# Kernel tuning notes

Measured on AMD Instinct MI355X. Metric: run time of the kernel, lower is better.

## Reference

```python
import jax, jax.numpy as jnp
import numpy as np

N = 100000      # nodes
E = 1_600_000   # edges (avg degree 16)
IN, HID, OUT = 64, 64, 32


def setup_inputs() -> dict:
    key = jax.random.key(0)
    k1, k2, k3, k4, k5, k6 = jax.random.split(key, 6)
    x = jax.random.uniform(k1, (N, IN), dtype=jnp.float32)
    edge_index = jax.random.randint(k2, (2, E), 0, N, dtype=jnp.int32)
    # GCNConv weights (glorot-ish scale) and biases
    W1 = jax.random.normal(k3, (IN, HID), dtype=jnp.float32) * (1.0 / np.sqrt(IN))
    b1 = jnp.zeros((HID,), dtype=jnp.float32)
    W2 = jax.random.normal(k4, (HID, OUT), dtype=jnp.float32) * (1.0 / np.sqrt(HID))
    b2 = jnp.zeros((OUT,), dtype=jnp.float32)
    return {"x": x, "edge_index": edge_index, "W1": W1, "b1": b1, "W2": W2, "b2": b2}


def reference(x, edge_index, W1, b1, W2, b2):
    n = x.shape[0]
    # PyG GCNConv: add self-loops, symmetric deg^{-1/2} normalization
    loops = jnp.arange(n, dtype=edge_index.dtype)
    src = jnp.concatenate([edge_index[0], loops])  # message sources
    dst = jnp.concatenate([edge_index[1], loops])  # message targets
    ones = jnp.ones(src.shape[0], dtype=x.dtype)
    deg = jax.ops.segment_sum(ones, dst, num_segments=n)
    dinv = jnp.where(deg > 0, jax.lax.rsqrt(deg), 0.0)
    norm = dinv[src] * dinv[dst]  # [E+N]

    def gcn_conv(h, W, b):
        h = h @ W                          # [n, d_out]
        msg = h[src] * norm[:, None]       # gather + edge-normalize
        agg = jax.ops.segment_sum(msg, dst, num_segments=n)  # scatter-add
        return agg + b

    h = jax.nn.relu(gcn_conv(x, W1, b1))
    return gcn_conv(h, W2, b2)
```

## Files before the change

kernel.cpp:

```cpp
#include <hip/hip_runtime.h>
#include <hip/hip_fp16.h>


#define BSHIFT 8
#define BNODES 256
#define NB 256
#define CAP 5120

union H8 {
    uint4 u;
    __half2 h[4];
};

__device__ inline float2 u2f2(unsigned u) {
    union { unsigned x; __half2 h; } c;
    c.x = u;
    return __half22float2(c.h);
}
__device__ inline unsigned f2u(float a, float b) {
    union { unsigned x; __half2 h; } c;
    c.h = __floats2half2_rn(a, b);
    return c.x;
}

__global__ __launch_bounds__(256) void scatter_kernel(
    const int* __restrict__ src, const int* __restrict__ dst,
    int* __restrict__ cur, int* __restrict__ buf, int E) {
    __shared__ int h[512];
    __shared__ int curl[512];
    int t = threadIdx.x, b = blockIdx.x;
    for (int i = t; i < 512; i += 256) h[i] = 0;
    __syncthreads();
    int per = (E + NB - 1) / NB;
    int lo = b * per;
    int hi = min(lo + per, E);
    for (int i = lo + t; i < hi; i += 256) atomicAdd(&h[dst[i] >> BSHIFT], 1);
    __syncthreads();
    for (int i = t; i < 512; i += 256) {
        int c = h[i];
        curl[i] = c ? atomicAdd(&cur[i], c) : 0;
    }
    __syncthreads();
    for (int i = lo + t; i < hi; i += 256) {
        int d = dst[i];
        int bin = d >> BSHIFT;
        int loc = atomicAdd(&curl[bin], 1);
        if (loc < CAP)
            buf[(size_t)bin * CAP + loc] = (src[i] << BSHIFT) | (d & (BNODES - 1));
    }
}

__global__ __launch_bounds__(256) void bsortgemm1_kernel(
    const int* __restrict__ cur, int* __restrict__ buf,
    int2* __restrict__ off2, float* __restrict__ dinv,
    const float* __restrict__ x, const float* __restrict__ W1,
    __half* __restrict__ hsh, int N) {
    __shared__ int stage[CAP];
    __shared__ int h[BNODES];
    __shared__ int c2[BNODES];
    __shared__ float4 Ws[64 * 16];
    int t = threadIdx.x, b = blockIdx.x;
    int cnt = min(cur[b], CAP);
    int base = b * CAP;
    for (int i = t; i < cnt; i += 256) stage[i] = buf[base + i];
    h[t] = 0;
    __syncthreads();
    for (int i = t; i < cnt; i += 256)
        atomicAdd(&h[stage[i] & (BNODES - 1)], 1);
    __syncthreads();
    int deg = h[t];
#pragma unroll
    for (int d = 1; d < BNODES; d <<= 1) {
        int v = (t >= d) ? h[t - d] : 0;
        __syncthreads();
        h[t] += v;
        __syncthreads();
    }
    int excl = h[t] - deg;
    c2[t] = excl;
    int node = (b << BSHIFT) + t;
    bool valid = node < N;
    float di = rsqrtf((float)(deg + 1));
    if (valid) {
        off2[node] = make_int2(base + excl, base + excl + deg);
        dinv[node] = di;
    }
    __syncthreads();
    for (int i = t; i < cnt; i += 256) {
        int p = stage[i];
        int pos = atomicAdd(&c2[p & (BNODES - 1)], 1);
        buf[base + pos] = p >> BSHIFT;
    }
    const float4* W4 = (const float4*)W1;
    for (int i = t; i < 1024; i += 256) Ws[i] = W4[i];
    __syncthreads();
    if (!valid) return;
    const float4* xr = (const float4*)(x + (size_t)node * 64);
    float4 acc[16];
#pragma unroll
    for (int j = 0; j < 16; j++) acc[j] = make_float4(0.f, 0.f, 0.f, 0.f);
    for (int k4 = 0; k4 < 16; k4++) {
        float4 xv = xr[k4];
#pragma unroll
        for (int kk = 0; kk < 4; kk++) {
            float a = ((const float*)&xv)[kk];
            const float4* wr = &Ws[(k4 * 4 + kk) * 16];
#pragma unroll
            for (int j = 0; j < 16; j++) {
                float4 w = wr[j];
                acc[j].x += a * w.x; acc[j].y += a * w.y;
                acc[j].z += a * w.z; acc[j].w += a * w.w;
            }
        }
    }
    uint4* ha = (uint4*)(hsh + (size_t)node * 64);
#pragma unroll
    for (int j = 0; j < 8; j++) {
        H8 p;
        float4 v0 = acc[2 * j], v1 = acc[2 * j + 1];
        p.h[0] = __floats2half2_rn(v0.x * di, v0.y * di);
        p.h[1] = __floats2half2_rn(v0.z * di, v0.w * di);
        p.h[2] = __floats2half2_rn(v1.x * di, v1.y * di);
        p.h[3] = __floats2half2_rn(v1.z * di, v1.w * di);
        ha[j] = p.u;
    }
}

__global__ __launch_bounds__(256) void agg1gemm2_kernel(
    const uint4* __restrict__ hsh4, const int* __restrict__ ssrc,
    const int2* __restrict__ off2, const float* __restrict__ dinv,
    const float* __restrict__ b1, const float* __restrict__ W2,
    __half* __restrict__ gsh, int N) {
    __shared__ float4 Ws2[64 * 8];
    int t = threadIdx.x;
    const float4* W24 = (const float4*)W2;
    for (int i = t; i < 512; i += 256) Ws2[i] = W24[i];
    __syncthreads();
    int lane = t & 63;
    int wid = (blockIdx.x * 256 + t) >> 6;
    int node = wid * 8 + (lane >> 3);
    int fi = lane & 7;
    if (node >= N) return;
    int2 lh = off2[node];
    int lo = lh.x, hi = lh.y;
    float di = dinv[node];
    H8 sv;
    sv.u = hsh4[(size_t)node * 8 + fi];
    float2 a0 = __half22float2(sv.h[0]);
    float2 a1 = __half22float2(sv.h[1]);
    float2 a2 = __half22float2(sv.h[2]);
    float2 a3 = __half22float2(sv.h[3]);
    float2 c0 = make_float2(0.f, 0.f), c1 = make_float2(0.f, 0.f);
    float2 c2 = make_float2(0.f, 0.f), c3 = make_float2(0.f, 0.f);
    int hm1 = hi - 1;
    for (int e = lo; e < hi; e += 8) {
        int i0 = e, i1 = min(e + 1, hm1), i2 = min(e + 2, hm1),
            i3 = min(e + 3, hm1);
        int i4 = min(e + 4, hm1), i5 = min(e + 5, hm1), i6 = min(e + 6, hm1),
            i7 = min(e + 7, hm1);
        int s0 = __builtin_nontemporal_load(&ssrc[i0]);
        int s1 = __builtin_nontemporal_load(&ssrc[i1]);
        int s2 = __builtin_nontemporal_load(&ssrc[i2]);
        int s3 = __builtin_nontemporal_load(&ssrc[i3]);
        int s4 = __builtin_nontemporal_load(&ssrc[i4]);
        int s5 = __builtin_nontemporal_load(&ssrc[i5]);
        int s6 = __builtin_nontemporal_load(&ssrc[i6]);
        int s7 = __builtin_nontemporal_load(&ssrc[i7]);
        H8 v0, v1, v2, v3, v4, v5, v6, v7;
        v0.u = hsh4[(size_t)s0 * 8 + fi];
        v1.u = hsh4[(size_t)s1 * 8 + fi];
        v2.u = hsh4[(size_t)s2 * 8 + fi];
        v3.u = hsh4[(size_t)s3 * 8 + fi];
        v4.u = hsh4[(size_t)s4 * 8 + fi];
        v5.u = hsh4[(size_t)s5 * 8 + fi];
        v6.u = hsh4[(size_t)s6 * 8 + fi];
        v7.u = hsh4[(size_t)s7 * 8 + fi];
        float m1 = (e + 1 < hi) ? 1.f : 0.f;
        float m2 = (e + 2 < hi) ? 1.f : 0.f;
        float m3 = (e + 3 < hi) ? 1.f : 0.f;
        float m4 = (e + 4 < hi) ? 1.f : 0.f;
        float m5 = (e + 5 < hi) ? 1.f : 0.f;
        float m6 = (e + 6 < hi) ? 1.f : 0.f;
        float m7 = (e + 7 < hi) ? 1.f : 0.f;
#pragma unroll
        for (int q = 0; q < 4; q++) {
            float2* aA = (q == 0) ? &a0 : (q == 1) ? &a1 : (q == 2) ? &a2 : &a3;
            float2* cA = (q == 0) ? &c0 : (q == 1) ? &c1 : (q == 2) ? &c2 : &c3;
            float2 f0 = __half22float2(v0.h[q]);
            float2 f1 = __half22float2(v1.h[q]);
            float2 f2 = __half22float2(v2.h[q]);
            float2 f3 = __half22float2(v3.h[q]);
            float2 f4 = __half22float2(v4.h[q]);
            float2 f5 = __half22float2(v5.h[q]);
            float2 f6 = __half22float2(v6.h[q]);
            float2 f7 = __half22float2(v7.h[q]);
            aA->x += f0.x + m1 * f1.x + m2 * f2.x + m3 * f3.x;
            aA->y += f0.y + m1 * f1.y + m2 * f2.y + m3 * f3.y;
            cA->x += m4 * f4.x + m5 * f5.x + m6 * f6.x + m7 * f7.x;
            cA->y += m4 * f4.y + m5 * f5.y + m6 * f6.y + m7 * f7.y;
        }
    }
    float4 bl = ((const float4*)b1)[fi * 2];
    float4 bh = ((const float4*)b1)[fi * 2 + 1];
    float r0 = fmaxf((a0.x + c0.x) * di + bl.x, 0.f);
    float r1 = fmaxf((a0.y + c0.y) * di + bl.y, 0.f);
    float r2 = fmaxf((a1.x + c1.x) * di + bl.z, 0.f);
    float r3 = fmaxf((a1.y + c1.y) * di + bl.w, 0.f);
    float r4 = fmaxf((a2.x + c2.x) * di + bh.x, 0.f);
    float r5 = fmaxf((a2.y + c2.y) * di + bh.y, 0.f);
    float r6 = fmaxf((a3.x + c3.x) * di + bh.z, 0.f);
    float r7 = fmaxf((a3.y + c3.y) * di + bh.w, 0.f);
    unsigned pk0 = f2u(r0, r1), pk1 = f2u(r2, r3);
    unsigned pk2 = f2u(r4, r5), pk3 = f2u(r6, r7);
    float4 acc2 = make_float4(0.f, 0.f, 0.f, 0.f);
#pragma unroll
    for (int s = 0; s < 8; s++) {
        int sl = (fi + s) & 7;
        unsigned u0 = __shfl(pk0, sl, 8);
        unsigned u1 = __shfl(pk1, sl, 8);
        unsigned u2 = __shfl(pk2, sl, 8);
        unsigned u3 = __shfl(pk3, sl, 8);
        float2 f0 = u2f2(u0), f1 = u2f2(u1), f2 = u2f2(u2), f3 = u2f2(u3);
        const float4* wr = &Ws2[sl * 64 + fi];
        float4 w;
        w = wr[0];
        acc2.x += f0.x * w.x; acc2.y += f0.x * w.y;
        acc2.z += f0.x * w.z; acc2.w += f0.x * w.w;
        w = wr[8];
        acc2.x += f0.y * w.x; acc2.y += f0.y * w.y;
        acc2.z += f0.y * w.z; acc2.w += f0.y * w.w;
        w = wr[16];
        acc2.x += f1.x * w.x; acc2.y += f1.x * w.y;
        acc2.z += f1.x * w.z; acc2.w += f1.x * w.w;
        w = wr[24];
        acc2.x += f1.y * w.x; acc2.y += f1.y * w.y;
        acc2.z += f1.y * w.z; acc2.w += f1.y * w.w;
        w = wr[32];
        acc2.x += f2.x * w.x; acc2.y += f2.x * w.y;
        acc2.z += f2.x * w.z; acc2.w += f2.x * w.w;
        w = wr[40];
        acc2.x += f2.y * w.x; acc2.y += f2.y * w.y;
        acc2.z += f2.y * w.z; acc2.w += f2.y * w.w;
        w = wr[48];
        acc2.x += f3.x * w.x; acc2.y += f3.x * w.y;
        acc2.z += f3.x * w.z; acc2.w += f3.x * w.w;
        w = wr[56];
        acc2.x += f3.y * w.x; acc2.y += f3.y * w.y;
        acc2.z += f3.y * w.z; acc2.w += f3.y * w.w;
    }
    uint2 pg;
    pg.x = f2u(acc2.x * di, acc2.y * di);
    pg.y = f2u(acc2.z * di, acc2.w * di);
    ((uint2*)gsh)[(size_t)node * 8 + fi] = pg;
}

__global__ __launch_bounds__(256) void agg2_kernel(
    const uint4* __restrict__ gsh4, const int* __restrict__ ssrc,
    const int2* __restrict__ off2, const float* __restrict__ dinv,
    const float* __restrict__ b2, float4* __restrict__ out4, int N) {
    int lane = threadIdx.x & 63;
    int wid = (blockIdx.x * 256 + threadIdx.x) >> 6;
    int node = wid * 16 + (lane >> 2);
    int fi = lane & 3;
    if (node >= N) return;
    int2 lh = off2[node];
    int lo = lh.x, hi = lh.y;
    float di = dinv[node];
    H8 sv;
    sv.u = gsh4[(size_t)node * 4 + fi];
    float2 a0 = __half22float2(sv.h[0]);
    float2 a1 = __half22float2(sv.h[1]);
    float2 a2 = __half22float2(sv.h[2]);
    float2 a3 = __half22float2(sv.h[3]);
    float2 c0 = make_float2(0.f, 0.f), c1 = make_float2(0.f, 0.f);
    float2 c2 = make_float2(0.f, 0.f), c3 = make_float2(0.f, 0.f);
    int hm1 = hi - 1;
    for (int e = lo; e < hi; e += 8) {
        int i1 = min(e + 1, hm1), i2 = min(e + 2, hm1), i3 = min(e + 3, hm1);
        int i4 = min(e + 4, hm1), i5 = min(e + 5, hm1), i6 = min(e + 6, hm1),
            i7 = min(e + 7, hm1);
        int s0 = __builtin_nontemporal_load(&ssrc[e]);
        int s1 = __builtin_nontemporal_load(&ssrc[i1]);
        int s2 = __builtin_nontemporal_load(&ssrc[i2]);
        int s3 = __builtin_nontemporal_load(&ssrc[i3]);
        int s4 = __builtin_nontemporal_load(&ssrc[i4]);
        int s5 = __builtin_nontemporal_load(&ssrc[i5]);
        int s6 = __builtin_nontemporal_load(&ssrc[i6]);
        int s7 = __builtin_nontemporal_load(&ssrc[i7]);
        H8 v0, v1, v2, v3, v4, v5, v6, v7;
        v0.u = gsh4[(size_t)s0 * 4 + fi];
        v1.u = gsh4[(size_t)s1 * 4 + fi];
        v2.u = gsh4[(size_t)s2 * 4 + fi];
        v3.u = gsh4[(size_t)s3 * 4 + fi];
        v4.u = gsh4[(size_t)s4 * 4 + fi];
        v5.u = gsh4[(size_t)s5 * 4 + fi];
        v6.u = gsh4[(size_t)s6 * 4 + fi];
        v7.u = gsh4[(size_t)s7 * 4 + fi];
        float m1 = (e + 1 < hi) ? 1.f : 0.f;
        float m2 = (e + 2 < hi) ? 1.f : 0.f;
        float m3 = (e + 3 < hi) ? 1.f : 0.f;
        float m4 = (e + 4 < hi) ? 1.f : 0.f;
        float m5 = (e + 5 < hi) ? 1.f : 0.f;
        float m6 = (e + 6 < hi) ? 1.f : 0.f;
        float m7 = (e + 7 < hi) ? 1.f : 0.f;
#pragma unroll
        for (int q = 0; q < 4; q++) {
            float2* aA = (q == 0) ? &a0 : (q == 1) ? &a1 : (q == 2) ? &a2 : &a3;
            float2* cA = (q == 0) ? &c0 : (q == 1) ? &c1 : (q == 2) ? &c2 : &c3;
            float2 f0 = __half22float2(v0.h[q]);
            float2 f1 = __half22float2(v1.h[q]);
            float2 f2 = __half22float2(v2.h[q]);
            float2 f3 = __half22float2(v3.h[q]);
            float2 f4 = __half22float2(v4.h[q]);
            float2 f5 = __half22float2(v5.h[q]);
            float2 f6 = __half22float2(v6.h[q]);
            float2 f7 = __half22float2(v7.h[q]);
            aA->x += f0.x + m1 * f1.x + m2 * f2.x + m3 * f3.x;
            aA->y += f0.y + m1 * f1.y + m2 * f2.y + m3 * f3.y;
            cA->x += m4 * f4.x + m5 * f5.x + m6 * f6.x + m7 * f7.x;
            cA->y += m4 * f4.y + m5 * f5.y + m6 * f6.y + m7 * f7.y;
        }
    }
    float4 bl = ((const float4*)b2)[fi * 2];
    float4 bh = ((const float4*)b2)[fi * 2 + 1];
    float4 r0, r1;
    r0.x = (a0.x + c0.x) * di + bl.x;
    r0.y = (a0.y + c0.y) * di + bl.y;
    r0.z = (a1.x + c1.x) * di + bl.z;
    r0.w = (a1.y + c1.y) * di + bl.w;
    r1.x = (a2.x + c2.x) * di + bh.x;
    r1.y = (a2.y + c2.y) * di + bh.y;
    r1.z = (a3.x + c3.x) * di + bh.z;
    r1.w = (a3.y + c3.y) * di + bh.w;
    out4[(size_t)node * 8 + fi * 2 + 0] = r0;
    out4[(size_t)node * 8 + fi * 2 + 1] = r1;
}

extern "C" void kernel_launch(void* const* d_in, const int* in_sizes, int n_in,
                              void* d_out, int out_size, void* d_ws,
                              size_t ws_size, hipStream_t stream) {
    const float* x  = (const float*)d_in[0];
    const int* ei   = (const int*)d_in[1];
    const float* W1 = (const float*)d_in[2];
    const float* b1 = (const float*)d_in[3];
    const float* W2 = (const float*)d_in[4];
    const float* b2 = (const float*)d_in[5];
    int N = in_sizes[0] / 64;
    int E = in_sizes[1] / 2;
    const int* src = ei;
    const int* dst = ei + E;
    int B = (N + BNODES - 1) >> BSHIFT;

    char* ws = (char*)d_ws;
    size_t o = 0;
    auto align16 = [&o]() { o = (o + 15) & ~(size_t)15; };
    int* cur    = (int*)(ws + o); o += 512 * 4; align16();
    int* buf    = (int*)(ws + o); o += (size_t)B * CAP * 4; align16();
    int2* off2  = (int2*)(ws + o); o += (size_t)N * 8; align16();
    float* dinv = (float*)(ws + o); o += (size_t)N * 4; align16();
    __half* hsh = (__half*)(ws + o); o += (size_t)N * 64 * 2; align16();
    __half* gsh = (__half*)(ws + o); o += (size_t)N * 32 * 2; align16();
    float* outp = (float*)d_out;

    hipMemsetAsync(cur, 0, 512 * 4, stream);
    scatter_kernel<<<NB, 256, 0, stream>>>(src, dst, cur, buf, E);
    bsortgemm1_kernel<<<B, 256, 0, stream>>>(cur, buf, off2, dinv, x, W1, hsh,
                                             N);
    agg1gemm2_kernel<<<(N + 31) / 32, 256, 0, stream>>>(
        (const uint4*)hsh, buf, off2, dinv, b1, W2, gsh, N);
    agg2_kernel<<<(N + 63) / 64, 256, 0, stream>>>(
        (const uint4*)gsh, buf, off2, dinv, b2, (float4*)outp, N);
}
```

Before: 208.1 us.

## Sub-sort neighbor lists by source window for gather locality

Sorts each destination node's incoming edges into eight source-index windows and records per-window counts packed into bytes. Both aggregation kernels then iterate window by window, so lanes in a wave gather from nearby source rows at the same time, improving cache hit rates. In exchange, each window segment is processed with its own masked 8-wide loop, adding padding iterations and control overhead. The byte-packed counts also assume fewer than 256 edges per window per node.

```diff
diff --git a/kernel.cpp b/kernel.cpp
--- a/kernel.cpp
+++ b/kernel.cpp
@@ -6,6 +6,7 @@
 #define BNODES 256
 #define NB 256
 #define CAP 5120
+#define WSHIFT 14
 
 union H8 {
     uint4 u;
@@ -53,44 +54,69 @@
 __global__ __launch_bounds__(256) void bsortgemm1_kernel(
     const int* __restrict__ cur, int* __restrict__ buf,
     int2* __restrict__ off2, float* __restrict__ dinv,
-    const float* __restrict__ x, const float* __restrict__ W1,
-    __half* __restrict__ hsh, int N) {
+    uint2* __restrict__ wlen, const float* __restrict__ x,
+    const float* __restrict__ W1, __half* __restrict__ hsh, int N) {
     __shared__ int stage[CAP];
-    __shared__ int h[BNODES];
-    __shared__ int c2[BNODES];
-    __shared__ float4 Ws[64 * 16];
+    __shared__ int h2[2048];
+    __shared__ int curs[2048];
+    __shared__ int sblk[256];
     int t = threadIdx.x, b = blockIdx.x;
     int cnt = min(cur[b], CAP);
     int base = b * CAP;
     for (int i = t; i < cnt; i += 256) stage[i] = buf[base + i];
-    h[t] = 0;
-    __syncthreads();
-    for (int i = t; i < cnt; i += 256)
-        atomicAdd(&h[stage[i] & (BNODES - 1)], 1);
-    __syncthreads();
-    int deg = h[t];
-#pragma unroll
-    for (int d = 1; d < BNODES; d <<= 1) {
-        int v = (t >= d) ? h[t - d] : 0;
+    for (int i = t; i < 2048; i += 256) h2[i] = 0;
+    __syncthreads();
+    for (int i = t; i < cnt; i += 256) {
+        int p = stage[i];
+        int key = ((p & 255) << 3) | (p >> (BSHIFT + WSHIFT));
+        atomicAdd(&h2[key], 1);
+    }
+    __syncthreads();
+    int c0 = h2[t * 8 + 0], c1 = h2[t * 8 + 1], c2 = h2[t * 8 + 2],
+        c3 = h2[t * 8 + 3];
+    int c4 = h2[t * 8 + 4], c5 = h2[t * 8 + 5], c6 = h2[t * 8 + 6],
+        c7 = h2[t * 8 + 7];
+    int deg = c0 + c1 + c2 + c3 + c4 + c5 + c6 + c7;
+    sblk[t] = deg;
+    __syncthreads();
+#pragma unroll
+    for (int d = 1; d < 256; d <<= 1) {
+        int v = (t >= d) ? sblk[t - d] : 0;
         __syncthreads();
-        h[t] += v;
+        sblk[t] += v;
         __syncthreads();
     }
-    int excl = h[t] - deg;
-    c2[t] = excl;
+    int excl = sblk[t] - deg;
+    int run = excl;
+    curs[t * 8 + 0] = run; run += c0;
+    curs[t * 8 + 1] = run; run += c1;
+    curs[t * 8 + 2] = run; run += c2;
+    curs[t * 8 + 3] = run; run += c3;
+    curs[t * 8 + 4] = run; run += c4;
+    curs[t * 8 + 5] = run; run += c5;
+    curs[t * 8 + 6] = run; run += c6;
+    curs[t * 8 + 7] = run;
     int node = (b << BSHIFT) + t;
     bool valid = node < N;
     float di = rsqrtf((float)(deg + 1));
     if (valid) {
         off2[node] = make_int2(base + excl, base + excl + deg);
         dinv[node] = di;
+        unsigned wx = (unsigned)c0 | ((unsigned)c1 << 8) |
+                      ((unsigned)c2 << 16) | ((unsigned)c3 << 24);
+        unsigned wy = (unsigned)c4 | ((unsigned)c5 << 8) |
+                      ((unsigned)c6 << 16) | ((unsigned)c7 << 24);
+        wlen[node] = make_uint2(wx, wy);
     }
     __syncthreads();
     for (int i = t; i < cnt; i += 256) {
         int p = stage[i];
-        int pos = atomicAdd(&c2[p & (BNODES - 1)], 1);
+        int key = ((p & 255) << 3) | (p >> (BSHIFT + WSHIFT));
+        int pos = atomicAdd(&curs[key], 1);
         buf[base + pos] = p >> BSHIFT;
     }
+    __syncthreads();
+    float4* Ws = (float4*)stage;
     const float4* W4 = (const float4*)W1;
     for (int i = t; i < 1024; i += 256) Ws[i] = W4[i];
     __syncthreads();
@@ -129,8 +155,8 @@
 __global__ __launch_bounds__(256) void agg1gemm2_kernel(
     const uint4* __restrict__ hsh4, const int* __restrict__ ssrc,
     const int2* __restrict__ off2, const float* __restrict__ dinv,
-    const float* __restrict__ b1, const float* __restrict__ W2,
-    __half* __restrict__ gsh, int N) {
+    const uint2* __restrict__ wlen, const float* __restrict__ b1,
+    const float* __restrict__ W2, __half* __restrict__ gsh, int N) {
     __shared__ float4 Ws2[64 * 8];
     int t = threadIdx.x;
     const float4* W24 = (const float4*)W2;
@@ -142,8 +168,10 @@
     int fi = lane & 7;
     if (node >= N) return;
     int2 lh = off2[node];
-    int lo = lh.x, hi = lh.y;
     float di = dinv[node];
+    uint2 wl = wlen[node];
+    unsigned long long wlu =
+        (((unsigned long long)wl.y) << 32) | (unsigned long long)wl.x;
     H8 sv;
     sv.u = hsh4[(size_t)node * 8 + fi];
     float2 a0 = __half22float2(sv.h[0]);
@@ -152,53 +180,63 @@
     float2 a3 = __half22float2(sv.h[3]);
     float2 c0 = make_float2(0.f, 0.f), c1 = make_float2(0.f, 0.f);
     float2 c2 = make_float2(0.f, 0.f), c3 = make_float2(0.f, 0.f);
-    int hm1 = hi - 1;
-    for (int e = lo; e < hi; e += 8) {
-        int i0 = e, i1 = min(e + 1, hm1), i2 = min(e + 2, hm1),
-            i3 = min(e + 3, hm1);
-        int i4 = min(e + 4, hm1), i5 = min(e + 5, hm1), i6 = min(e + 6, hm1),
-            i7 = min(e + 7, hm1);
-        int s0 = __builtin_nontemporal_load(&ssrc[i0]);
-        int s1 = __builtin_nontemporal_load(&ssrc[i1]);
-        int s2 = __builtin_nontemporal_load(&ssrc[i2]);
-        int s3 = __builtin_nontemporal_load(&ssrc[i3]);
-        int s4 = __builtin_nontemporal_load(&ssrc[i4]);
-        int s5 = __builtin_nontemporal_load(&ssrc[i5]);
-        int s6 = __builtin_nontemporal_load(&ssrc[i6]);
-        int s7 = __builtin_nontemporal_load(&ssrc[i7]);
-        H8 v0, v1, v2, v3, v4, v5, v6, v7;
-        v0.u = hsh4[(size_t)s0 * 8 + fi];
-        v1.u = hsh4[(size_t)s1 * 8 + fi];
-        v2.u = hsh4[(size_t)s2 * 8 + fi];
-        v3.u = hsh4[(size_t)s3 * 8 + fi];
-        v4.u = hsh4[(size_t)s4 * 8 + fi];
-        v5.u = hsh4[(size_t)s5 * 8 + fi];
-        v6.u = hsh4[(size_t)s6 * 8 + fi];
-        v7.u = hsh4[(size_t)s7 * 8 + fi];
-        float m1 = (e + 1 < hi) ? 1.f : 0.f;
-        float m2 = (e + 2 < hi) ? 1.f : 0.f;
-        float m3 = (e + 3 < hi) ? 1.f : 0.f;
-        float m4 = (e + 4 < hi) ? 1.f : 0.f;
-        float m5 = (e + 5 < hi) ? 1.f : 0.f;
-        float m6 = (e + 6 < hi) ? 1.f : 0.f;
-        float m7 = (e + 7 < hi) ? 1.f : 0.f;
-#pragma unroll
-        for (int q = 0; q < 4; q++) {
-            float2* aA = (q == 0) ? &a0 : (q == 1) ? &a1 : (q == 2) ? &a2 : &a3;
-            float2* cA = (q == 0) ? &c0 : (q == 1) ? &c1 : (q == 2) ? &c2 : &c3;
-            float2 f0 = __half22float2(v0.h[q]);
-            float2 f1 = __half22float2(v1.h[q]);
-            float2 f2 = __half22float2(v2.h[q]);
-            float2 f3 = __half22float2(v3.h[q]);
-            float2 f4 = __half22float2(v4.h[q]);
-            float2 f5 = __half22float2(v5.h[q]);
-            float2 f6 = __half22float2(v6.h[q]);
-            float2 f7 = __half22float2(v7.h[q]);
-            aA->x += f0.x + m1 * f1.x + m2 * f2.x + m3 * f3.x;
-            aA->y += f0.y + m1 * f1.y + m2 * f2.y + m3 * f3.y;
-            cA->x += m4 * f4.x + m5 * f5.x + m6 * f6.x + m7 * f7.x;
-            cA->y += m4 * f4.y + m5 * f5.y + m6 * f6.y + m7 * f7.y;
+    int e = lh.x;
+#pragma unroll 1
+    for (int w = 0; w < 8; w++) {
+        int len = (int)((wlu >> (8 * w)) & 255ULL);
+        if (len == 0) continue;
+        int seg_end = e + len;
+        int hm1 = seg_end - 1;
+        for (; e < seg_end; e += 8) {
+            int i1 = min(e + 1, hm1), i2 = min(e + 2, hm1),
+                i3 = min(e + 3, hm1);
+            int i4 = min(e + 4, hm1), i5 = min(e + 5, hm1),
+                i6 = min(e + 6, hm1), i7 = min(e + 7, hm1);
+            int s0 = __builtin_nontemporal_load(&ssrc[e]);
+            int s1 = __builtin_nontemporal_load(&ssrc[i1]);
+            int s2 = __builtin_nontemporal_load(&ssrc[i2]);
+            int s3 = __builtin_nontemporal_load(&ssrc[i3]);
+            int s4 = __builtin_nontemporal_load(&ssrc[i4]);
+            int s5 = __builtin_nontemporal_load(&ssrc[i5]);
+            int s6 = __builtin_nontemporal_load(&ssrc[i6]);
+            int s7 = __builtin_nontemporal_load(&ssrc[i7]);
+            H8 v0, v1, v2, v3, v4, v5, v6, v7;
+            v0.u = hsh4[(size_t)s0 * 8 + fi];
+            v1.u = hsh4[(size_t)s1 * 8 + fi];
+            v2.u = hsh4[(size_t)s2 * 8 + fi];
+            v3.u = hsh4[(size_t)s3 * 8 + fi];
+            v4.u = hsh4[(size_t)s4 * 8 + fi];
+            v5.u = hsh4[(size_t)s5 * 8 + fi];
+            v6.u = hsh4[(size_t)s6 * 8 + fi];
+            v7.u = hsh4[(size_t)s7 * 8 + fi];
+            float m1 = (e + 1 < seg_end) ? 1.f : 0.f;
+            float m2 = (e + 2 < seg_end) ? 1.f : 0.f;
+            float m3 = (e + 3 < seg_end) ? 1.f : 0.f;
+            float m4 = (e + 4 < seg_end) ? 1.f : 0.f;
+            float m5 = (e + 5 < seg_end) ? 1.f : 0.f;
+            float m6 = (e + 6 < seg_end) ? 1.f : 0.f;
+            float m7 = (e + 7 < seg_end) ? 1.f : 0.f;
+#pragma unroll
+            for (int q = 0; q < 4; q++) {
+                float2* aA = (q == 0) ? &a0 : (q == 1) ? &a1
+                                      : (q == 2) ? &a2 : &a3;
+                float2* cA = (q == 0) ? &c0 : (q == 1) ? &c1
+                                      : (q == 2) ? &c2 : &c3;
+                float2 f0 = __half22float2(v0.h[q]);
+                float2 f1 = __half22float2(v1.h[q]);
+                float2 f2 = __half22float2(v2.h[q]);
+                float2 f3 = __half22float2(v3.h[q]);
+                float2 f4 = __half22float2(v4.h[q]);
+                float2 f5 = __half22float2(v5.h[q]);
+                float2 f6 = __half22float2(v6.h[q]);
+                float2 f7 = __half22float2(v7.h[q]);
+                aA->x += f0.x + m1 * f1.x + m2 * f2.x + m3 * f3.x;
+                aA->y += f0.y + m1 * f1.y + m2 * f2.y + m3 * f3.y;
+                cA->x += m4 * f4.x + m5 * f5.x + m6 * f6.x + m7 * f7.x;
+                cA->y += m4 * f4.y + m5 * f5.y + m6 * f6.y + m7 * f7.y;
+            }
         }
+        e = seg_end;
     }
     float4 bl = ((const float4*)b1)[fi * 2];
     float4 bh = ((const float4*)b1)[fi * 2 + 1];
@@ -257,15 +295,18 @@
 __global__ __launch_bounds__(256) void agg2_kernel(
     const uint4* __restrict__ gsh4, const int* __restrict__ ssrc,
     const int2* __restrict__ off2, const float* __restrict__ dinv,
-    const float* __restrict__ b2, float4* __restrict__ out4, int N) {
+    const uint2* __restrict__ wlen, const float* __restrict__ b2,
+    float4* __restrict__ out4, int N) {
     int lane = threadIdx.x & 63;
     int wid = (blockIdx.x * 256 + threadIdx.x) >> 6;
     int node = wid * 16 + (lane >> 2);
     int fi = lane & 3;
     if (node >= N) return;
     int2 lh = off2[node];
-    int lo = lh.x, hi = lh.y;
     float di = dinv[node];
+    uint2 wl = wlen[node];
+    unsigned long long wlu =
+        (((unsigned long long)wl.y) << 32) | (unsigned long long)wl.x;
     H8 sv;
     sv.u = gsh4[(size_t)node * 4 + fi];
     float2 a0 = __half22float2(sv.h[0]);
@@ -274,52 +315,63 @@
     float2 a3 = __half22float2(sv.h[3]);
     float2 c0 = make_float2(0.f, 0.f), c1 = make_float2(0.f, 0.f);
     float2 c2 = make_float2(0.f, 0.f), c3 = make_float2(0.f, 0.f);
-    int hm1 = hi - 1;
-    for (int e = lo; e < hi; e += 8) {
-        int i1 = min(e + 1, hm1), i2 = min(e + 2, hm1), i3 = min(e + 3, hm1);
-        int i4 = min(e + 4, hm1), i5 = min(e + 5, hm1), i6 = min(e + 6, hm1),
-            i7 = min(e + 7, hm1);
-        int s0 = __builtin_nontemporal_load(&ssrc[e]);
-        int s1 = __builtin_nontemporal_load(&ssrc[i1]);
-        int s2 = __builtin_nontemporal_load(&ssrc[i2]);
-        int s3 = __builtin_nontemporal_load(&ssrc[i3]);
-        int s4 = __builtin_nontemporal_load(&ssrc[i4]);
-        int s5 = __builtin_nontemporal_load(&ssrc[i5]);
-        int s6 = __builtin_nontemporal_load(&ssrc[i6]);
-        int s7 = __builtin_nontemporal_load(&ssrc[i7]);
-        H8 v0, v1, v2, v3, v4, v5, v6, v7;
-        v0.u = gsh4[(size_t)s0 * 4 + fi];
-        v1.u = gsh4[(size_t)s1 * 4 + fi];
-        v2.u = gsh4[(size_t)s2 * 4 + fi];
-        v3.u = gsh4[(size_t)s3 * 4 + fi];
-        v4.u = gsh4[(size_t)s4 * 4 + fi];
-        v5.u = gsh4[(size_t)s5 * 4 + fi];
-        v6.u = gsh4[(size_t)s6 * 4 + fi];
-        v7.u = gsh4[(size_t)s7 * 4 + fi];
-        float m1 = (e + 1 < hi) ? 1.f : 0.f;
-        float m2 = (e + 2 < hi) ? 1.f : 0.f;
-        float m3 = (e + 3 < hi) ? 1.f : 0.f;
-        float m4 = (e + 4 < hi) ? 1.f : 0.f;
-        float m5 = (e + 5 < hi) ? 1.f : 0.f;
-        float m6 = (e + 6 < hi) ? 1.f : 0.f;
-        float m7 = (e + 7 < hi) ? 1.f : 0.f;
-#pragma unroll
-        for (int q = 0; q < 4; q++) {
-            float2* aA = (q == 0) ? &a0 : (q == 1) ? &a1 : (q == 2) ? &a2 : &a3;
-            float2* cA = (q == 0) ? &c0 : (q == 1) ? &c1 : (q == 2) ? &c2 : &c3;
-            float2 f0 = __half22float2(v0.h[q]);
-            float2 f1 = __half22float2(v1.h[q]);
-            float2 f2 = __half22float2(v2.h[q]);
-            float2 f3 = __half22float2(v3.h[q]);
-            float2 f4 = __half22float2(v4.h[q]);
-            float2 f5 = __half22float2(v5.h[q]);
-            float2 f6 = __half22float2(v6.h[q]);
-            float2 f7 = __half22float2(v7.h[q]);
-            aA->x += f0.x + m1 * f1.x + m2 * f2.x + m3 * f3.x;
-            aA->y += f0.y + m1 * f1.y + m2 * f2.y + m3 * f3.y;
-            cA->x += m4 * f4.x + m5 * f5.x + m6 * f6.x + m7 * f7.x;
-            cA->y += m4 * f4.y + m5 * f5.y + m6 * f6.y + m7 * f7.y;
+    int e = lh.x;
+#pragma unroll 1
+    for (int w = 0; w < 8; w++) {
+        int len = (int)((wlu >> (8 * w)) & 255ULL);
+        if (len == 0) continue;
+        int seg_end = e + len;
+        int hm1 = seg_end - 1;
+        for (; e < seg_end; e += 8) {
+            int i1 = min(e + 1, hm1), i2 = min(e + 2, hm1),
+                i3 = min(e + 3, hm1);
+            int i4 = min(e + 4, hm1), i5 = min(e + 5, hm1),
+                i6 = min(e + 6, hm1), i7 = min(e + 7, hm1);
+            int s0 = __builtin_nontemporal_load(&ssrc[e]);
+            int s1 = __builtin_nontemporal_load(&ssrc[i1]);
+            int s2 = __builtin_nontemporal_load(&ssrc[i2]);
+            int s3 = __builtin_nontemporal_load(&ssrc[i3]);
+            int s4 = __builtin_nontemporal_load(&ssrc[i4]);
+            int s5 = __builtin_nontemporal_load(&ssrc[i5]);
+            int s6 = __builtin_nontemporal_load(&ssrc[i6]);
+            int s7 = __builtin_nontemporal_load(&ssrc[i7]);
+            H8 v0, v1, v2, v3, v4, v5, v6, v7;
+            v0.u = gsh4[(size_t)s0 * 4 + fi];
+            v1.u = gsh4[(size_t)s1 * 4 + fi];
+            v2.u = gsh4[(size_t)s2 * 4 + fi];
+            v3.u = gsh4[(size_t)s3 * 4 + fi];
+            v4.u = gsh4[(size_t)s4 * 4 + fi];
+            v5.u = gsh4[(size_t)s5 * 4 + fi];
+            v6.u = gsh4[(size_t)s6 * 4 + fi];
+            v7.u = gsh4[(size_t)s7 * 4 + fi];
+            float m1 = (e + 1 < seg_end) ? 1.f : 0.f;
+            float m2 = (e + 2 < seg_end) ? 1.f : 0.f;
+            float m3 = (e + 3 < seg_end) ? 1.f : 0.f;
+            float m4 = (e + 4 < seg_end) ? 1.f : 0.f;
+            float m5 = (e + 5 < seg_end) ? 1.f : 0.f;
+            float m6 = (e + 6 < seg_end) ? 1.f : 0.f;
+            float m7 = (e + 7 < seg_end) ? 1.f : 0.f;
+#pragma unroll
+            for (int q = 0; q < 4; q++) {
+                float2* aA = (q == 0) ? &a0 : (q == 1) ? &a1
+                                      : (q == 2) ? &a2 : &a3;
+                float2* cA = (q == 0) ? &c0 : (q == 1) ? &c1
+                                      : (q == 2) ? &c2 : &c3;
+                float2 f0 = __half22float2(v0.h[q]);
+                float2 f1 = __half22float2(v1.h[q]);
+                float2 f2 = __half22float2(v2.h[q]);
+                float2 f3 = __half22float2(v3.h[q]);
+                float2 f4 = __half22float2(v4.h[q]);
+                float2 f5 = __half22float2(v5.h[q]);
+                float2 f6 = __half22float2(v6.h[q]);
+                float2 f7 = __half22float2(v7.h[q]);
+                aA->x += f0.x + m1 * f1.x + m2 * f2.x + m3 * f3.x;
+                aA->y += f0.y + m1 * f1.y + m2 * f2.y + m3 * f3.y;
+                cA->x += m4 * f4.x + m5 * f5.x + m6 * f6.x + m7 * f7.x;
+                cA->y += m4 * f4.y + m5 * f5.y + m6 * f6.y + m7 * f7.y;
+            }
         }
+        e = seg_end;
     }
     float4 bl = ((const float4*)b2)[fi * 2];
     float4 bh = ((const float4*)b2)[fi * 2 + 1];
@@ -358,16 +410,17 @@
     int* buf    = (int*)(ws + o); o += (size_t)B * CAP * 4; align16();
     int2* off2  = (int2*)(ws + o); o += (size_t)N * 8; align16();
     float* dinv = (float*)(ws + o); o += (size_t)N * 4; align16();
+    uint2* wlen = (uint2*)(ws + o); o += (size_t)N * 8; align16();
     __half* hsh = (__half*)(ws + o); o += (size_t)N * 64 * 2; align16();
     __half* gsh = (__half*)(ws + o); o += (size_t)N * 32 * 2; align16();
     float* outp = (float*)d_out;
 
     hipMemsetAsync(cur, 0, 512 * 4, stream);
     scatter_kernel<<<NB, 256, 0, stream>>>(src, dst, cur, buf, E);
-    bsortgemm1_kernel<<<B, 256, 0, stream>>>(cur, buf, off2, dinv, x, W1, hsh,
-                                             N);
+    bsortgemm1_kernel<<<B, 256, 0, stream>>>(cur, buf, off2, dinv, wlen, x,
+                                             W1, hsh, N);
     agg1gemm2_kernel<<<(N + 31) / 32, 256, 0, stream>>>(
-        (const uint4*)hsh, buf, off2, dinv, b1, W2, gsh, N);
+        (const uint4*)hsh, buf, off2, dinv, wlen, b1, W2, gsh, N);
     agg2_kernel<<<(N + 63) / 64, 256, 0, stream>>>(
-        (const uint4*)gsh, buf, off2, dinv, b2, (float4*)outp, N);
-}
+        (const uint4*)gsh, buf, off2, dinv, wlen, b2, (float4*)outp, N);
+}
```

Result: slower. 241.8 us (+16.2%).

## Split bucket sort from GEMM1 and register-tile GEMM1 as 4x16 per thread

Applied to the files above, without the earlier changes.

The fused sort+GEMM1 kernel is split into a sort-only kernel and a separate GEMM1 kernel. GEMM1 now has each thread compute 4 rows by 16 output columns instead of one full 64-wide row. This cuts the accumulator registers from 64 to 64 per thread but with 4x reuse of each W load, and spreads row loads across 4 threads. It is meant to improve occupancy and shared-memory reuse in GEMM1, at the cost of an extra kernel launch and re-reading dinv from global memory.

```diff
diff --git a/kernel.cpp b/kernel.cpp
--- a/kernel.cpp
+++ b/kernel.cpp
@@ -50,15 +50,12 @@
     }
 }
 
-__global__ __launch_bounds__(256) void bsortgemm1_kernel(
+__global__ __launch_bounds__(256) void bsort_kernel(
     const int* __restrict__ cur, int* __restrict__ buf,
-    int2* __restrict__ off2, float* __restrict__ dinv,
-    const float* __restrict__ x, const float* __restrict__ W1,
-    __half* __restrict__ hsh, int N) {
+    int2* __restrict__ off2, float* __restrict__ dinv, int N) {
     __shared__ int stage[CAP];
     __shared__ int h[BNODES];
     __shared__ int c2[BNODES];
-    __shared__ float4 Ws[64 * 16];
     int t = threadIdx.x, b = blockIdx.x;
     int cnt = min(cur[b], CAP);
     int base = b * CAP;
@@ -79,11 +76,9 @@
     int excl = h[t] - deg;
     c2[t] = excl;
     int node = (b << BSHIFT) + t;
-    bool valid = node < N;
-    float di = rsqrtf((float)(deg + 1));
-    if (valid) {
+    if (node < N) {
         off2[node] = make_int2(base + excl, base + excl + deg);
-        dinv[node] = di;
+        dinv[node] = rsqrtf((float)(deg + 1));
     }
     __syncthreads();
     for (int i = t; i < cnt; i += 256) {
@@ -91,38 +86,68 @@
         int pos = atomicAdd(&c2[p & (BNODES - 1)], 1);
         buf[base + pos] = p >> BSHIFT;
     }
+}
+
+__global__ __launch_bounds__(256) void gemm1_kernel(
+    const float* __restrict__ x, const float* __restrict__ W1,
+    const float* __restrict__ dinv, __half* __restrict__ hsh, int N) {
+    __shared__ float4 Ws[64 * 16];
+    int t = threadIdx.x;
     const float4* W4 = (const float4*)W1;
     for (int i = t; i < 1024; i += 256) Ws[i] = W4[i];
     __syncthreads();
-    if (!valid) return;
-    const float4* xr = (const float4*)(x + (size_t)node * 64);
-    float4 acc[16];
-#pragma unroll
-    for (int j = 0; j < 16; j++) acc[j] = make_float4(0.f, 0.f, 0.f, 0.f);
+    int c = t & 3;
+    int rg = t >> 2;
+    int r0 = blockIdx.x * 256 + rg * 4;
+    if (r0 >= N) return;
+    int nm1 = N - 1;
+    float4 acc[4][4];
+#pragma unroll
+    for (int r = 0; r < 4; r++)
+#pragma unroll
+        for (int j = 0; j < 4; j++) acc[r][j] = make_float4(0.f, 0.f, 0.f, 0.f);
+    const float4* x4 = (const float4*)x;
     for (int k4 = 0; k4 < 16; k4++) {
-        float4 xv = xr[k4];
+        float4 xv[4];
+#pragma unroll
+        for (int r = 0; r < 4; r++)
+            xv[r] = x4[(size_t)min(r0 + r, nm1) * 16 + k4];
 #pragma unroll
         for (int kk = 0; kk < 4; kk++) {
-            float a = ((const float*)&xv)[kk];
-            const float4* wr = &Ws[(k4 * 4 + kk) * 16];
-#pragma unroll
-            for (int j = 0; j < 16; j++) {
-                float4 w = wr[j];
-                acc[j].x += a * w.x; acc[j].y += a * w.y;
-                acc[j].z += a * w.z; acc[j].w += a * w.w;
+            const float4* wr = &Ws[(k4 * 4 + kk) * 16 + c * 4];
+            float4 w0 = wr[0], w1 = wr[1], w2 = wr[2], w3 = wr[3];
+#pragma unroll
+            for (int r = 0; r < 4; r++) {
+                float a = (kk == 0) ? xv[r].x : (kk == 1) ? xv[r].y
+                          : (kk == 2) ? xv[r].z : xv[r].w;
+                acc[r][0].x += a * w0.x; acc[r][0].y += a * w0.y;
+                acc[r][0].z += a * w0.z; acc[r][0].w += a * w0.w;
+                acc[r][1].x += a * w1.x; acc[r][1].y += a * w1.y;
+                acc[r][1].z += a * w1.z; acc[r][1].w += a * w1.w;
+                acc[r][2].x += a * w2.x; acc[r][2].y += a * w2.y;
+                acc[r][2].z += a * w2.z; acc[r][2].w += a * w2.w;
+                acc[r][3].x += a * w3.x; acc[r][3].y += a * w3.y;
+                acc[r][3].z += a * w3.z; acc[r][3].w += a * w3.w;
             }
         }
     }
-    uint4* ha = (uint4*)(hsh + (size_t)node * 64);
-#pragma unroll
-    for (int j = 0; j < 8; j++) {
-        H8 p;
-        float4 v0 = acc[2 * j], v1 = acc[2 * j + 1];
-        p.h[0] = __floats2half2_rn(v0.x * di, v0.y * di);
-        p.h[1] = __floats2half2_rn(v0.z * di, v0.w * di);
-        p.h[2] = __floats2half2_rn(v1.x * di, v1.y * di);
-        p.h[3] = __floats2half2_rn(v1.z * di, v1.w * di);
-        ha[j] = p.u;
+#pragma unroll
+    for (int r = 0; r < 4; r++) {
+        int row = r0 + r;
+        if (row >= N) break;
+        float di = dinv[row];
+        uint4* ha = (uint4*)(hsh + (size_t)row * 64);
+        H8 p0, p1;
+        p0.h[0] = __floats2half2_rn(acc[r][0].x * di, acc[r][0].y * di);
+        p0.h[1] = __floats2half2_rn(acc[r][0].z * di, acc[r][0].w * di);
+        p0.h[2] = __floats2half2_rn(acc[r][1].x * di, acc[r][1].y * di);
+        p0.h[3] = __floats2half2_rn(acc[r][1].z * di, acc[r][1].w * di);
+        p1.h[0] = __floats2half2_rn(acc[r][2].x * di, acc[r][2].y * di);
+        p1.h[1] = __floats2half2_rn(acc[r][2].z * di, acc[r][2].w * di);
+        p1.h[2] = __floats2half2_rn(acc[r][3].x * di, acc[r][3].y * di);
+        p1.h[3] = __floats2half2_rn(acc[r][3].z * di, acc[r][3].w * di);
+        ha[c * 2 + 0] = p0.u;
+        ha[c * 2 + 1] = p1.u;
     }
 }
 
@@ -154,11 +179,10 @@
     float2 c2 = make_float2(0.f, 0.f), c3 = make_float2(0.f, 0.f);
     int hm1 = hi - 1;
     for (int e = lo; e < hi; e += 8) {
-        int i0 = e, i1 = min(e + 1, hm1), i2 = min(e + 2, hm1),
-            i3 = min(e + 3, hm1);
+        int i1 = min(e + 1, hm1), i2 = min(e + 2, hm1), i3 = min(e + 3, hm1);
         int i4 = min(e + 4, hm1), i5 = min(e + 5, hm1), i6 = min(e + 6, hm1),
             i7 = min(e + 7, hm1);
-        int s0 = __builtin_nontemporal_load(&ssrc[i0]);
+        int s0 = __builtin_nontemporal_load(&ssrc[e]);
         int s1 = __builtin_nontemporal_load(&ssrc[i1]);
         int s2 = __builtin_nontemporal_load(&ssrc[i2]);
         int s3 = __builtin_nontemporal_load(&ssrc[i3]);
@@ -364,8 +388,8 @@
 
     hipMemsetAsync(cur, 0, 512 * 4, stream);
     scatter_kernel<<<NB, 256, 0, stream>>>(src, dst, cur, buf, E);
-    bsortgemm1_kernel<<<B, 256, 0, stream>>>(cur, buf, off2, dinv, x, W1, hsh,
-                                             N);
+    bsort_kernel<<<B, 256, 0, stream>>>(cur, buf, off2, dinv, N);
+    gemm1_kernel<<<(N + 255) / 256, 256, 0, stream>>>(x, W1, dinv, hsh, N);
     agg1gemm2_kernel<<<(N + 31) / 32, 256, 0, stream>>>(
         (const uint4*)hsh, buf, off2, dinv, b1, W2, gsh, N);
     agg2_kernel<<<(N + 63) / 64, 256, 0, stream>>>(
```

After: 207.4 us. Within noise of the previous version (-0.4%).
